# Kernel tuning notes

Measured on AMD Instinct MI355X. Metric: run time of the kernel, lower is better.

## Reference

```python
import jax, jax.numpy as jnp
import numpy as np

EPS_BN = 1e-5
EPS_W = 1e-8


def _bn(x, g, b, m, v):
    # x: [B, N, C]; params: [C] (inference-mode batchnorm)
    return g * (x - m) * jax.lax.rsqrt(v + EPS_BN) + b


def setup_inputs() -> dict:
    key = jax.random.key(0)
    ks = jax.random.split(key, 24)
    B, N, S = 16, 4096, 1024
    C1, C2 = 128, 256            # points1 / points2 channels
    CIN, COUT = C1 + C2, 128     # in_channel, out_channel

    def w(k, shape, std=0.02):
        return (jax.random.normal(k, shape, jnp.float32) * std)

    def bn_params(k, c):
        k1, k2, k3, k4 = jax.random.split(k, 4)
        return (1.0 + 0.1 * jax.random.normal(k1, (c,), jnp.float32),  # gamma
                0.1 * jax.random.normal(k2, (c,), jnp.float32),        # beta
                0.1 * jax.random.normal(k3, (c,), jnp.float32),        # running mean
                0.5 + jax.random.uniform(k4, (c,), jnp.float32))       # running var

    fg, fb, fm, fv = bn_params(ks[4], COUT)
    g1, b1, m1, v1 = bn_params(ks[5], COUT)
    g2, b2, m2, v2 = bn_params(ks[6], COUT)
    return {
        "xyz1": jax.random.uniform(ks[0], (B, N, 3), jnp.float32),
        "xyz2": jax.random.uniform(ks[1], (B, S, 3), jnp.float32),
        "points1": jax.random.normal(ks[2], (B, C1, N), jnp.float32),
        "points2": jax.random.normal(ks[3], (B, C2, S), jnp.float32),
        "fuse_w": w(ks[7], (COUT, CIN)), "fuse_b": jnp.zeros((COUT,), jnp.float32),
        "fuse_g": fg, "fuse_beta": fb, "fuse_m": fm, "fuse_v": fv,
        "c1_w": w(ks[8], (COUT, COUT)), "c1_b": jnp.zeros((COUT,), jnp.float32),
        "bn1_g": g1, "bn1_b": b1, "bn1_m": m1, "bn1_v": v1,
        "c2_w": w(ks[9], (COUT, COUT)), "c2_b": jnp.zeros((COUT,), jnp.float32),
        "bn2_g": g2, "bn2_b": b2, "bn2_m": m2, "bn2_v": v2,
    }


def reference(xyz1, xyz2, points1, points2,
              fuse_w, fuse_b, fuse_g, fuse_beta, fuse_m, fuse_v,
              c1_w, c1_b, bn1_g, bn1_b, bn1_m, bn1_v,
              c2_w, c2_b, bn2_g, bn2_b, bn2_m, bn2_v):
    B, N, _ = xyz1.shape
    pts1 = jnp.swapaxes(points1, 1, 2)   # [B, N, C1]
    pts2 = jnp.swapaxes(points2, 1, 2)   # [B, S, C2]

    # squared pairwise distances [B, N, S]
    dists = (jnp.sum(xyz1 ** 2, -1)[:, :, None]
             + jnp.sum(xyz2 ** 2, -1)[:, None, :]
             - 2.0 * jnp.einsum('bnc,bsc->bns', xyz1, xyz2))

    # 3 nearest neighbors (smallest distances)
    neg_d3, idx = jax.lax.top_k(-dists, 3)          # [B, N, 3]
    d3 = -neg_d3
    recip = 1.0 / (d3 + EPS_W)
    weight = recip / jnp.sum(recip, axis=2, keepdims=True)  # [B, N, 3]

    gathered = jax.vmap(lambda p, i: p[i])(pts2, idx)        # [B, N, 3, C2]
    interp = jnp.sum(gathered * weight[..., None], axis=2)   # [B, N, C2]

    x = jnp.concatenate([pts1, interp], axis=-1)             # [B, N, CIN]

    # fuse: 1x1 conv + BN + ReLU
    x = jax.nn.relu(_bn(jnp.einsum('bnc,oc->bno', x, fuse_w) + fuse_b,
                        fuse_g, fuse_beta, fuse_m, fuse_v))

    # residual block: conv-BN-ReLU -> conv-BN, add skip, ReLU
    h = jax.nn.relu(_bn(jnp.einsum('bnc,oc->bno', x, c1_w) + c1_b,
                        bn1_g, bn1_b, bn1_m, bn1_v))
    y = _bn(jnp.einsum('bnc,oc->bno', h, c2_w) + c2_b,
            bn2_g, bn2_b, bn2_m, bn2_v)
    out = jax.nn.relu(y + x)                                 # [B, N, COUT]
    return jnp.swapaxes(out, 1, 2)                           # [B, COUT, N]
```

## Files before the change

### kernel.cpp

```cpp
#include <hip/hip_runtime.h>
#include <hip/hip_bf16.h>

#define BB 16
#define NN 4096
#define SS 1024
#define C1 128
#define C2 256
#define CIN 384
#define CO 128

typedef __bf16 bf16x8 __attribute__((ext_vector_type(8)));
typedef float f32x4 __attribute__((ext_vector_type(4)));

__global__ __launch_bounds__(256) void knn_kernel(
    const float* __restrict__ xyz1, const float* __restrict__ xyz2,
    int* __restrict__ idx4, float* __restrict__ w4)
{
    __shared__ float4 pts[SS];
    const int b = blockIdx.y;
    const float* p2 = xyz2 + (size_t)b * SS * 3;
    for (int i = threadIdx.x; i < SS; i += 256) {
        float x = p2[i * 3 + 0], y = p2[i * 3 + 1], z = p2[i * 3 + 2];
        pts[i] = make_float4(x, y, z, x * x + y * y + z * z);
    }
    __syncthreads();

    const int n = blockIdx.x * 256 + threadIdx.x;
    const float* p1 = xyz1 + ((size_t)b * NN + n) * 3;
    const float x = p1[0], y = p1[1], z = p1[2];
    const float s1 = x * x + y * y + z * z;

    float d0 = 3.4e38f, d1 = 3.4e38f, d2 = 3.4e38f, d3 = 3.4e38f;
    int i0 = 0, i1 = 0, i2 = 0, i3 = 0;
    #pragma unroll 4
    for (int s = 0; s < SS; ++s) {
        float4 p = pts[s];
        float d = s1 + p.w - 2.0f * (x * p.x + y * p.y + z * p.z);
        bool lt0 = d < d0, lt1 = d < d1, lt2 = d < d2, lt3 = d < d3;
        float nd3 = lt2 ? d2 : (lt3 ? d : d3); int ni3 = lt2 ? i2 : (lt3 ? s : i3);
        float nd2 = lt1 ? d1 : (lt2 ? d : d2); int ni2 = lt1 ? i1 : (lt2 ? s : i2);
        float nd1 = lt0 ? d0 : (lt1 ? d : d1); int ni1 = lt0 ? i0 : (lt1 ? s : i1);
        d0 = lt0 ? d : d0;                     i0 = lt0 ? s : i0;
        d1 = nd1; i1 = ni1; d2 = nd2; i2 = ni2; d3 = nd3; i3 = ni3;
    }
    float r0 = 1.0f / (d0 + 1e-8f);
    float r1 = 1.0f / (d1 + 1e-8f);
    float r2 = 1.0f / (d2 + 1e-8f);
    float rs = r0 + r1 + r2;
    bool tie = (d2 == d3);
    size_t base = ((size_t)b * NN + n) * 4;
    idx4[base + 0] = i0; idx4[base + 1] = i1;
    idx4[base + 2] = i2; idx4[base + 3] = i3;
    w4[base + 0] = r0 / rs; w4[base + 1] = r1 / rs;
    w4[base + 2] = r2 / rs; w4[base + 3] = tie ? -1.0f : 0.0f;
}

__global__ __launch_bounds__(256) void p2t_kernel(
    const float* __restrict__ p2, float* __restrict__ p2t)
{
    __shared__ float tile[64][65];
    const int b = blockIdx.z;
    const int s0 = blockIdx.x * 64, c0 = blockIdx.y * 64;
    for (int i = threadIdx.x; i < 64 * 64; i += 256) {
        int s = i & 63, c = i >> 6;
        tile[c][s] = p2[((size_t)b * C2 + c0 + c) * SS + s0 + s];
    }
    __syncthreads();
    for (int i = threadIdx.x; i < 64 * 64; i += 256) {
        int c = i & 63, s = i >> 6;
        p2t[((size_t)b * SS + s0 + s) * C2 + c0 + c] = tile[c][s];
    }
}

__global__ __launch_bounds__(256) void tie_eval_kernel(
    const float* __restrict__ p2t, const float* __restrict__ points1,
    const int* __restrict__ idx4, float* __restrict__ w4,
    const float* __restrict__ fw, const float* __restrict__ fb,
    const float* __restrict__ fg, const float* __restrict__ fbt,
    const float* __restrict__ fm, const float* __restrict__ fv,
    const float* __restrict__ w1m, const float* __restrict__ b1,
    const float* __restrict__ g1, const float* __restrict__ bt1,
    const float* __restrict__ m1, const float* __restrict__ v1,
    const float* __restrict__ w2m, const float* __restrict__ b2,
    const float* __restrict__ g2, const float* __restrict__ bt2,
    const float* __restrict__ m2, const float* __restrict__ v2)
{
    __shared__ float Xs[4][2][CIN];
    __shared__ float XT[4][2][CO];
    __shared__ float Hs[4][2][CO];
    const int wave = threadIdx.x >> 6, lane = threadIdx.x & 63;
    const int n = blockIdx.x * 4 + wave;
    const int b = blockIdx.y;
    const size_t base = ((size_t)b * NN + n) * 4;
    if (w4[base + 3] != -1.0f) return;

    const int i0 = idx4[base + 0], i1 = idx4[base + 1];
    const int i2 = idx4[base + 2], i3 = idx4[base + 3];
    const float w0 = w4[base + 0], w1 = w4[base + 1], w2 = w4[base + 2];
    const float* P = p2t + (size_t)b * SS * C2;

    for (int c = lane; c < C1; c += 64) {
        float v = points1[((size_t)b * C1 + c) * NN + n];
        Xs[wave][0][c] = v; Xs[wave][1][c] = v;
    }
    for (int c = lane; c < C2; c += 64) {
        float f0 = P[(size_t)i0 * C2 + c], f1 = P[(size_t)i1 * C2 + c];
        float f2 = P[(size_t)i2 * C2 + c], f3 = P[(size_t)i3 * C2 + c];
        float bs = w0 * f0 + w1 * f1;
        Xs[wave][0][C1 + c] = bs + w2 * f2;
        Xs[wave][1][C1 + c] = bs + w2 * f3;
    }
    #pragma unroll
    for (int k = 0; k < 2; ++k) {
        int oc = lane + 64 * k;
        float alo = fb[oc], ahi = fb[oc];
        for (int c = 0; c < CIN; ++c) {
            float wv = fw[(size_t)oc * CIN + c];
            alo += wv * Xs[wave][0][c];
            ahi += wv * Xs[wave][1][c];
        }
        float s = fg[oc] * (1.0f / sqrtf(fv[oc] + 1e-5f));
        XT[wave][0][oc] = fmaxf(s * (alo - fm[oc]) + fbt[oc], 0.0f);
        XT[wave][1][oc] = fmaxf(s * (ahi - fm[oc]) + fbt[oc], 0.0f);
    }
    #pragma unroll
    for (int k = 0; k < 2; ++k) {
        int oc = lane + 64 * k;
        float alo = b1[oc], ahi = b1[oc];
        for (int c = 0; c < CO; ++c) {
            float wv = w1m[(size_t)oc * CO + c];
            alo += wv * XT[wave][0][c];
            ahi += wv * XT[wave][1][c];
        }
        float s = g1[oc] * (1.0f / sqrtf(v1[oc] + 1e-5f));
        Hs[wave][0][oc] = fmaxf(s * (alo - m1[oc]) + bt1[oc], 0.0f);
        Hs[wave][1][oc] = fmaxf(s * (ahi - m1[oc]) + bt1[oc], 0.0f);
    }
    float e = 0.0f;
    #pragma unroll
    for (int k = 0; k < 2; ++k) {
        int oc = lane + 64 * k;
        float alo = b2[oc], ahi = b2[oc];
        for (int c = 0; c < CO; ++c) {
            float wv = w2m[(size_t)oc * CO + c];
            alo += wv * Hs[wave][0][c];
            ahi += wv * Hs[wave][1][c];
        }
        float s = g2[oc] * (1.0f / sqrtf(v2[oc] + 1e-5f));
        float olo = fmaxf(s * (alo - m2[oc]) + bt2[oc] + XT[wave][0][oc], 0.0f);
        float ohi = fmaxf(s * (ahi - m2[oc]) + bt2[oc] + XT[wave][1][oc], 0.0f);
        e = fmaxf(e, fabsf(olo - ohi));
    }
    for (int off = 32; off; off >>= 1) e = fmaxf(e, __shfl_xor(e, off));
    if (lane == 0) {
        if (e > 0.085f) { w4[base + 3] = 0.0f; }
        else { w4[base + 2] = 0.5f * w2; w4[base + 3] = 0.5f * w2; }
    }
}

__global__ __launch_bounds__(256) void buildx_kernel(
    const float* __restrict__ points1,
    const float* __restrict__ p2t,
    const int* __restrict__ idx4, const float* __restrict__ w4,
    float* __restrict__ X)
{
    __shared__ float t1[128][66];
    const int b = blockIdx.y;
    const int n0 = blockIdx.x * 64;
    for (int i = threadIdx.x; i < 128 * 64; i += 256) {
        int j = i & 63, c = i >> 6;
        t1[c][j] = points1[((size_t)b * C1 + c) * NN + n0 + j];
    }
    __syncthreads();
    for (int i = threadIdx.x; i < 128 * 64; i += 256) {
        int c = i & 127, j = i >> 7;
        X[((size_t)b * NN + n0 + j) * CIN + c] = t1[c][j];
    }
    for (int i = threadIdx.x; i < 64 * C2; i += 256) {
        int c = i & 255, j = i >> 8;
        int n = n0 + j;
        size_t ib = ((size_t)b * NN + n) * 4;
        int s0 = idx4[ib + 0], s1 = idx4[ib + 1];
        int s2 = idx4[ib + 2], s3 = idx4[ib + 3];
        float w0 = w4[ib + 0], w1 = w4[ib + 1];
        float w2 = w4[ib + 2], w3 = w4[ib + 3];
        const float* base = p2t + (size_t)b * SS * C2;
        float v = w0 * base[(size_t)s0 * C2 + c]
                + w1 * base[(size_t)s1 * C2 + c]
                + w2 * base[(size_t)s2 * C2 + c]
                + w3 * base[(size_t)s3 * C2 + c];
        X[((size_t)b * NN + n) * CIN + C1 + c] = v;
    }
}

template<int K, int MODE>
__global__ __launch_bounds__(256) void gemm_bn_kernel(
    const float* __restrict__ A,
    const float* __restrict__ W,
    const float* __restrict__ cb,  const float* __restrict__ gg,
    const float* __restrict__ bbta, const float* __restrict__ mm,
    const float* __restrict__ vv,
    const float* __restrict__ skip,
    float* __restrict__ out)
{
    __shared__ __attribute__((aligned(16))) __hip_bfloat16 wh[128 * 40];
    __shared__ __attribute__((aligned(16))) __hip_bfloat16 wl[128 * 40];
    __shared__ float s_s[128], s_t[128];
    const int tid = threadIdx.x;
    if (tid < 128) {
        float s = gg[tid] * (1.0f / sqrtf(vv[tid] + 1e-5f));
        float t = (cb[tid] - mm[tid]) * s + bbta[tid];
        s_s[tid] = s; s_t[tid] = t;
    }
    const int wave = tid >> 6, lane = tid & 63;
    const int m = lane & 15, q = lane >> 4;
    const size_t r0 = (size_t)blockIdx.x * 64 + wave * 16;

    f32x4 acc[8] = {};
    const float* arow = A + (r0 + m) * K + q * 8;

    for (int kk = 0; kk < K; kk += 32) {
        __syncthreads();
        int c = tid;
        #pragma unroll
        for (int rep = 0; rep < 2; ++rep, c += 256) {
            int row = c >> 2, qq = c & 3;
            const float4 wa = *(const float4*)&W[(size_t)row * K + kk + qq * 8];
            const float4 wb = *(const float4*)&W[(size_t)row * K + kk + qq * 8 + 4];
            float wf[8] = {wa.x, wa.y, wa.z, wa.w, wb.x, wb.y, wb.z, wb.w};
            bf16x8 vh, vl;
            #pragma unroll
            for (int t = 0; t < 8; ++t) {
                __bf16 h = (__bf16)wf[t];
                vh[t] = h;
                vl[t] = (__bf16)(wf[t] - (float)h);
            }
            *(bf16x8*)&wh[row * 40 + qq * 8] = vh;
            *(bf16x8*)&wl[row * 40 + qq * 8] = vl;
        }
        __syncthreads();
        const float4 aa = *(const float4*)(arow + kk);
        const float4 ab = *(const float4*)(arow + kk + 4);
        float af[8] = {aa.x, aa.y, aa.z, aa.w, ab.x, ab.y, ab.z, ab.w};
        bf16x8 a_hi, a_lo;
        #pragma unroll
        for (int t = 0; t < 8; ++t) {
            __bf16 h = (__bf16)af[t];
            a_hi[t] = h;
            a_lo[t] = (__bf16)(af[t] - (float)h);
        }
        #pragma unroll
        for (int ot = 0; ot < 8; ++ot) {
            bf16x8 bh = *(const bf16x8*)&wh[(ot * 16 + m) * 40 + q * 8];
            bf16x8 bl = *(const bf16x8*)&wl[(ot * 16 + m) * 40 + q * 8];
            acc[ot] = __builtin_amdgcn_mfma_f32_16x16x32_bf16(a_hi, bh, acc[ot], 0, 0, 0);
            acc[ot] = __builtin_amdgcn_mfma_f32_16x16x32_bf16(a_lo, bh, acc[ot], 0, 0, 0);
            acc[ot] = __builtin_amdgcn_mfma_f32_16x16x32_bf16(a_hi, bl, acc[ot], 0, 0, 0);
        }
    }

    #pragma unroll
    for (int ot = 0; ot < 8; ++ot) {
        int col = ot * 16 + m;
        float sc = s_s[col], sh = s_t[col];
        #pragma unroll
        for (int r = 0; r < 4; ++r) {
            size_t row = r0 + q * 4 + r;
            float val = acc[ot][r] * sc + sh;
            if (MODE == 0) {
                val = fmaxf(val, 0.0f);
                out[row * 128 + col] = val;
            } else {
                val += skip[row * 128 + col];
                val = fmaxf(val, 0.0f);
                int bidx = (int)(row >> 12);
                int n = (int)(row & 4095);
                out[((size_t)bidx * 128 + col) * NN + n] = val;
            }
        }
    }
}

extern "C" void kernel_launch(void* const* d_in, const int* in_sizes, int n_in,
                              void* d_out, int out_size, void* d_ws, size_t ws_size,
                              hipStream_t stream) {
    const float* xyz1    = (const float*)d_in[0];
    const float* xyz2    = (const float*)d_in[1];
    const float* points1 = (const float*)d_in[2];
    const float* points2 = (const float*)d_in[3];
    const float* fuse_w  = (const float*)d_in[4];
    const float* fuse_b  = (const float*)d_in[5];
    const float* fuse_g  = (const float*)d_in[6];
    const float* fuse_bt = (const float*)d_in[7];
    const float* fuse_m  = (const float*)d_in[8];
    const float* fuse_v  = (const float*)d_in[9];
    const float* c1_w    = (const float*)d_in[10];
    const float* c1_b    = (const float*)d_in[11];
    const float* bn1_g   = (const float*)d_in[12];
    const float* bn1_b   = (const float*)d_in[13];
    const float* bn1_m   = (const float*)d_in[14];
    const float* bn1_v   = (const float*)d_in[15];
    const float* c2_w    = (const float*)d_in[16];
    const float* c2_b    = (const float*)d_in[17];
    const float* bn2_g   = (const float*)d_in[18];
    const float* bn2_b   = (const float*)d_in[19];
    const float* bn2_m   = (const float*)d_in[20];
    const float* bn2_v   = (const float*)d_in[21];

    char* ws = (char*)d_ws;
    int*   idx4 = (int*)(ws);
    float* w4   = (float*)(ws + 1048576);
    float* p2t  = (float*)(ws + 2097152);
    float* X    = (float*)(ws + 18874368);
    float* Y0   = (float*)(ws + 119537664);
    float* H    = (float*)(ws + 153092096);

    knn_kernel<<<dim3(NN / 256, BB), 256, 0, stream>>>(xyz1, xyz2, idx4, w4);
    p2t_kernel<<<dim3(SS / 64, C2 / 64, BB), 256, 0, stream>>>(points2, p2t);
    tie_eval_kernel<<<dim3(NN / 4, BB), 256, 0, stream>>>(
        p2t, points1, idx4, w4,
        fuse_w, fuse_b, fuse_g, fuse_bt, fuse_m, fuse_v,
        c1_w, c1_b, bn1_g, bn1_b, bn1_m, bn1_v,
        c2_w, c2_b, bn2_g, bn2_b, bn2_m, bn2_v);
    buildx_kernel<<<dim3(NN / 64, BB), 256, 0, stream>>>(points1, p2t, idx4, w4, X);

    const int mblocks = (BB * NN) / 64;
    gemm_bn_kernel<CIN, 0><<<mblocks, 256, 0, stream>>>(
        X, fuse_w, fuse_b, fuse_g, fuse_bt, fuse_m, fuse_v, nullptr, Y0);
    gemm_bn_kernel<CO, 0><<<mblocks, 256, 0, stream>>>(
        Y0, c1_w, c1_b, bn1_g, bn1_b, bn1_m, bn1_v, nullptr, H);
    gemm_bn_kernel<CO, 1><<<mblocks, 256, 0, stream>>>(
        H, c2_w, c2_b, bn2_g, bn2_b, bn2_m, bn2_v, Y0, (float*)d_out);
}
```

Measured before the change: 374.6 us.

## Pre-split operands into bf16 hi/lo, double GEMM row tile, coalesce transposed output

Weights are split into bf16 hi/lo pairs once in a new prep kernel, and the activations X, Y0 and H are stored as bf16 hi/lo pairs, so the GEMMs no longer convert fp32 to bf16 on every tile. Each wave now computes 32 rows instead of 16, which reuses each LDS weight fragment twice. The final GEMM transposes its output through shared memory so the [B,C,N] writes are coalesced. The intermediate traffic stays the same size (two bf16 halves per fp32 value), but it adds an extra launch and more accumulator registers, which may lower occupancy.

```diff
diff --git a/kernel.cpp b/kernel.cpp
--- a/kernel.cpp
+++ b/kernel.cpp
@@ -72,6 +72,22 @@
     }
 }
 
+__global__ __launch_bounds__(256) void wprep_kernel(
+    const float* __restrict__ fw, const float* __restrict__ w1,
+    const float* __restrict__ w2,
+    __bf16* __restrict__ Whf, __bf16* __restrict__ Wlf,
+    __bf16* __restrict__ Wh1, __bf16* __restrict__ Wl1,
+    __bf16* __restrict__ Wh2, __bf16* __restrict__ Wl2)
+{
+    int t = blockIdx.x * 256 + threadIdx.x;
+    float v; __bf16 *oh, *ol; int idx;
+    if (t < 49152)      { idx = t;         v = fw[idx]; oh = Whf; ol = Wlf; }
+    else if (t < 65536) { idx = t - 49152; v = w1[idx]; oh = Wh1; ol = Wl1; }
+    else                { idx = t - 65536; v = w2[idx]; oh = Wh2; ol = Wl2; }
+    __bf16 h = (__bf16)v;
+    oh[idx] = h; ol[idx] = (__bf16)(v - (float)h);
+}
+
 __global__ __launch_bounds__(256) void tie_eval_kernel(
     const float* __restrict__ p2t, const float* __restrict__ points1,
     const int* __restrict__ idx4, float* __restrict__ w4,
@@ -162,7 +178,7 @@
     const float* __restrict__ points1,
     const float* __restrict__ p2t,
     const int* __restrict__ idx4, const float* __restrict__ w4,
-    float* __restrict__ X)
+    __bf16* __restrict__ Xh, __bf16* __restrict__ Xl)
 {
     __shared__ float t1[128][66];
     const int b = blockIdx.y;
@@ -174,7 +190,10 @@
     __syncthreads();
     for (int i = threadIdx.x; i < 128 * 64; i += 256) {
         int c = i & 127, j = i >> 7;
-        X[((size_t)b * NN + n0 + j) * CIN + c] = t1[c][j];
+        float v = t1[c][j];
+        __bf16 h = (__bf16)v;
+        size_t o = ((size_t)b * NN + n0 + j) * CIN + c;
+        Xh[o] = h; Xl[o] = (__bf16)(v - (float)h);
     }
     for (int i = threadIdx.x; i < 64 * C2; i += 256) {
         int c = i & 255, j = i >> 8;
@@ -189,23 +208,27 @@
                 + w1 * base[(size_t)s1 * C2 + c]
                 + w2 * base[(size_t)s2 * C2 + c]
                 + w3 * base[(size_t)s3 * C2 + c];
-        X[((size_t)b * NN + n) * CIN + C1 + c] = v;
+        __bf16 h = (__bf16)v;
+        size_t o = ((size_t)b * NN + n) * CIN + C1 + c;
+        Xh[o] = h; Xl[o] = (__bf16)(v - (float)h);
     }
 }
 
 template<int K, int MODE>
 __global__ __launch_bounds__(256) void gemm_bn_kernel(
-    const float* __restrict__ A,
-    const float* __restrict__ W,
+    const __bf16* __restrict__ Ah, const __bf16* __restrict__ Al,
+    const __bf16* __restrict__ Wh, const __bf16* __restrict__ Wl,
     const float* __restrict__ cb,  const float* __restrict__ gg,
     const float* __restrict__ bbta, const float* __restrict__ mm,
     const float* __restrict__ vv,
-    const float* __restrict__ skip,
-    float* __restrict__ out)
-{
-    __shared__ __attribute__((aligned(16))) __hip_bfloat16 wh[128 * 40];
-    __shared__ __attribute__((aligned(16))) __hip_bfloat16 wl[128 * 40];
+    const __bf16* __restrict__ skiph, const __bf16* __restrict__ skipl,
+    __bf16* __restrict__ outh, __bf16* __restrict__ outl,
+    float* __restrict__ outf)
+{
+    __shared__ __attribute__((aligned(16))) __bf16 wls_h[128 * 40];
+    __shared__ __attribute__((aligned(16))) __bf16 wls_l[128 * 40];
     __shared__ float s_s[128], s_t[128];
+    __shared__ float tile[32][132];
     const int tid = threadIdx.x;
     if (tid < 128) {
         float s = gg[tid] * (1.0f / sqrtf(vv[tid] + 1e-5f));
@@ -214,68 +237,85 @@
     }
     const int wave = tid >> 6, lane = tid & 63;
     const int m = lane & 15, q = lane >> 4;
-    const size_t r0 = (size_t)blockIdx.x * 64 + wave * 16;
-
-    f32x4 acc[8] = {};
-    const float* arow = A + (r0 + m) * K + q * 8;
-
+    const size_t r0 = (size_t)blockIdx.x * 128 + wave * 32;
+
+    f32x4 acc[2][8] = {};
+    const __bf16* pAh = Ah + (r0 + m) * (size_t)K + q * 8;
+    const __bf16* pAl = Al + (r0 + m) * (size_t)K + q * 8;
+
+    const int wrow = tid >> 1, whf = tid & 1;
     for (int kk = 0; kk < K; kk += 32) {
         __syncthreads();
-        int c = tid;
-        #pragma unroll
-        for (int rep = 0; rep < 2; ++rep, c += 256) {
-            int row = c >> 2, qq = c & 3;
-            const float4 wa = *(const float4*)&W[(size_t)row * K + kk + qq * 8];
-            const float4 wb = *(const float4*)&W[(size_t)row * K + kk + qq * 8 + 4];
-            float wf[8] = {wa.x, wa.y, wa.z, wa.w, wb.x, wb.y, wb.z, wb.w};
-            bf16x8 vh, vl;
-            #pragma unroll
-            for (int t = 0; t < 8; ++t) {
-                __bf16 h = (__bf16)wf[t];
-                vh[t] = h;
-                vl[t] = (__bf16)(wf[t] - (float)h);
-            }
-            *(bf16x8*)&wh[row * 40 + qq * 8] = vh;
-            *(bf16x8*)&wl[row * 40 + qq * 8] = vl;
+        {
+            size_t g = (size_t)wrow * K + kk + whf * 16;
+            int lo = wrow * 40 + whf * 16;
+            *(uint4*)&wls_h[lo]     = *(const uint4*)&Wh[g];
+            *(uint4*)&wls_h[lo + 8] = *(const uint4*)&Wh[g + 8];
+            *(uint4*)&wls_l[lo]     = *(const uint4*)&Wl[g];
+            *(uint4*)&wls_l[lo + 8] = *(const uint4*)&Wl[g + 8];
         }
         __syncthreads();
-        const float4 aa = *(const float4*)(arow + kk);
-        const float4 ab = *(const float4*)(arow + kk + 4);
-        float af[8] = {aa.x, aa.y, aa.z, aa.w, ab.x, ab.y, ab.z, ab.w};
-        bf16x8 a_hi, a_lo;
-        #pragma unroll
-        for (int t = 0; t < 8; ++t) {
-            __bf16 h = (__bf16)af[t];
-            a_hi[t] = h;
-            a_lo[t] = (__bf16)(af[t] - (float)h);
-        }
+        bf16x8 ah0 = *(const bf16x8*)(pAh + kk);
+        bf16x8 al0 = *(const bf16x8*)(pAl + kk);
+        bf16x8 ah1 = *(const bf16x8*)(pAh + 16 * (size_t)K + kk);
+        bf16x8 al1 = *(const bf16x8*)(pAl + 16 * (size_t)K + kk);
         #pragma unroll
         for (int ot = 0; ot < 8; ++ot) {
-            bf16x8 bh = *(const bf16x8*)&wh[(ot * 16 + m) * 40 + q * 8];
-            bf16x8 bl = *(const bf16x8*)&wl[(ot * 16 + m) * 40 + q * 8];
-            acc[ot] = __builtin_amdgcn_mfma_f32_16x16x32_bf16(a_hi, bh, acc[ot], 0, 0, 0);
-            acc[ot] = __builtin_amdgcn_mfma_f32_16x16x32_bf16(a_lo, bh, acc[ot], 0, 0, 0);
-            acc[ot] = __builtin_amdgcn_mfma_f32_16x16x32_bf16(a_hi, bl, acc[ot], 0, 0, 0);
-        }
-    }
-
-    #pragma unroll
-    for (int ot = 0; ot < 8; ++ot) {
-        int col = ot * 16 + m;
-        float sc = s_s[col], sh = s_t[col];
+            bf16x8 bh = *(const bf16x8*)&wls_h[(ot * 16 + m) * 40 + q * 8];
+            bf16x8 bl = *(const bf16x8*)&wls_l[(ot * 16 + m) * 40 + q * 8];
+            acc[0][ot] = __builtin_amdgcn_mfma_f32_16x16x32_bf16(ah0, bh, acc[0][ot], 0, 0, 0);
+            acc[0][ot] = __builtin_amdgcn_mfma_f32_16x16x32_bf16(al0, bh, acc[0][ot], 0, 0, 0);
+            acc[0][ot] = __builtin_amdgcn_mfma_f32_16x16x32_bf16(ah0, bl, acc[0][ot], 0, 0, 0);
+            acc[1][ot] = __builtin_amdgcn_mfma_f32_16x16x32_bf16(ah1, bh, acc[1][ot], 0, 0, 0);
+            acc[1][ot] = __builtin_amdgcn_mfma_f32_16x16x32_bf16(al1, bh, acc[1][ot], 0, 0, 0);
+            acc[1][ot] = __builtin_amdgcn_mfma_f32_16x16x32_bf16(ah1, bl, acc[1][ot], 0, 0, 0);
+        }
+    }
+
+    if (MODE == 0) {
         #pragma unroll
-        for (int r = 0; r < 4; ++r) {
-            size_t row = r0 + q * 4 + r;
-            float val = acc[ot][r] * sc + sh;
-            if (MODE == 0) {
-                val = fmaxf(val, 0.0f);
-                out[row * 128 + col] = val;
-            } else {
-                val += skip[row * 128 + col];
-                val = fmaxf(val, 0.0f);
-                int bidx = (int)(row >> 12);
-                int n = (int)(row & 4095);
-                out[((size_t)bidx * 128 + col) * NN + n] = val;
+        for (int rt = 0; rt < 2; ++rt) {
+            #pragma unroll
+            for (int ot = 0; ot < 8; ++ot) {
+                int col = ot * 16 + m;
+                float sc = s_s[col], sh = s_t[col];
+                #pragma unroll
+                for (int r = 0; r < 4; ++r) {
+                    size_t row = r0 + rt * 16 + q * 4 + r;
+                    float val = fmaxf(acc[rt][ot][r] * sc + sh, 0.0f);
+                    __bf16 h = (__bf16)val;
+                    outh[row * 128 + col] = h;
+                    outl[row * 128 + col] = (__bf16)(val - (float)h);
+                }
+            }
+        }
+    } else {
+        const int bidx = (int)(((size_t)blockIdx.x * 128) >> 12);
+        const int nbase = (int)(((size_t)blockIdx.x * 128) & 4095);
+        for (int cc = 0; cc < 4; ++cc) {
+            __syncthreads();
+            #pragma unroll
+            for (int oo = 0; oo < 2; ++oo) {
+                int ot = cc * 2 + oo;
+                int col = ot * 16 + m;
+                float sc = s_s[col], sh = s_t[col];
+                #pragma unroll
+                for (int rt = 0; rt < 2; ++rt) {
+                    #pragma unroll
+                    for (int r = 0; r < 4; ++r) {
+                        int lrow = wave * 32 + rt * 16 + q * 4 + r;
+                        size_t row = (size_t)blockIdx.x * 128 + lrow;
+                        float val = acc[rt][ot][r] * sc + sh;
+                        val += (float)skiph[row * 128 + col] + (float)skipl[row * 128 + col];
+                        val = fmaxf(val, 0.0f);
+                        tile[oo * 16 + m][lrow] = val;
+                    }
+                }
+            }
+            __syncthreads();
+            for (int c2 = tid >> 7; c2 < 32; c2 += 2) {
+                int nn_ = tid & 127;
+                outf[((size_t)bidx * 128 + cc * 32 + c2) * NN + nbase + nn_] = tile[c2][nn_];
             }
         }
     }
@@ -308,27 +348,41 @@
     const float* bn2_v   = (const float*)d_in[21];
 
     char* ws = (char*)d_ws;
-    int*   idx4 = (int*)(ws);
-    float* w4   = (float*)(ws + 1048576);
-    float* p2t  = (float*)(ws + 2097152);
-    float* X    = (float*)(ws + 18874368);
-    float* Y0   = (float*)(ws + 119537664);
-    float* H    = (float*)(ws + 153092096);
+    int*    idx4 = (int*)(ws);
+    float*  w4   = (float*)(ws + 1048576);
+    float*  p2t  = (float*)(ws + 2097152);
+    __bf16* Xh   = (__bf16*)(ws + 18874368);
+    __bf16* Xl   = (__bf16*)(ws + 69206016);
+    __bf16* Y0h  = (__bf16*)(ws + 119537664);
+    __bf16* Y0l  = (__bf16*)(ws + 136314880);
+    __bf16* Hh   = (__bf16*)(ws + 153092096);
+    __bf16* Hl   = (__bf16*)(ws + 169869312);
+    __bf16* Whf  = (__bf16*)(ws + 186646528);
+    __bf16* Wlf  = (__bf16*)(ws + 186744832);
+    __bf16* Wh1  = (__bf16*)(ws + 186843136);
+    __bf16* Wl1  = (__bf16*)(ws + 186875904);
+    __bf16* Wh2  = (__bf16*)(ws + 186908672);
+    __bf16* Wl2  = (__bf16*)(ws + 186941440);
 
     knn_kernel<<<dim3(NN / 256, BB), 256, 0, stream>>>(xyz1, xyz2, idx4, w4);
     p2t_kernel<<<dim3(SS / 64, C2 / 64, BB), 256, 0, stream>>>(points2, p2t);
+    wprep_kernel<<<320, 256, 0, stream>>>(fuse_w, c1_w, c2_w,
+                                          Whf, Wlf, Wh1, Wl1, Wh2, Wl2);
     tie_eval_kernel<<<dim3(NN / 4, BB), 256, 0, stream>>>(
         p2t, points1, idx4, w4,
         fuse_w, fuse_b, fuse_g, fuse_bt, fuse_m, fuse_v,
         c1_w, c1_b, bn1_g, bn1_b, bn1_m, bn1_v,
         c2_w, c2_b, bn2_g, bn2_b, bn2_m, bn2_v);
-    buildx_kernel<<<dim3(NN / 64, BB), 256, 0, stream>>>(points1, p2t, idx4, w4, X);
-
-    const int mblocks = (BB * NN) / 64;
-    gemm_bn_kernel<CIN, 0><<<mblocks, 256, 0, stream>>>(
-        X, fuse_w, fuse_b, fuse_g, fuse_bt, fuse_m, fuse_v, nullptr, Y0);
-    gemm_bn_kernel<CO, 0><<<mblocks, 256, 0, stream>>>(
-        Y0, c1_w, c1_b, bn1_g, bn1_b, bn1_m, bn1_v, nullptr, H);
-    gemm_bn_kernel<CO, 1><<<mblocks, 256, 0, stream>>>(
-        H, c2_w, c2_b, bn2_g, bn2_b, bn2_m, bn2_v, Y0, (float*)d_out);
-}
+    buildx_kernel<<<dim3(NN / 64, BB), 256, 0, stream>>>(points1, p2t, idx4, w4, Xh, Xl);
+
+    const int gblocks = (BB * NN) / 128;
+    gemm_bn_kernel<CIN, 0><<<gblocks, 256, 0, stream>>>(
+        Xh, Xl, Whf, Wlf, fuse_b, fuse_g, fuse_bt, fuse_m, fuse_v,
+        nullptr, nullptr, Y0h, Y0l, nullptr);
+    gemm_bn_kernel<CO, 0><<<gblocks, 256, 0, stream>>>(
+        Y0h, Y0l, Wh1, Wl1, c1_b, bn1_g, bn1_b, bn1_m, bn1_v,
+        nullptr, nullptr, Hh, Hl, nullptr);
+    gemm_bn_kernel<CO, 1><<<gblocks, 256, 0, stream>>>(
+        Hh, Hl, Wh2, Wl2, c2_b, bn2_g, bn2_b, bn2_m, bn2_v,
+        Y0h, Y0l, nullptr, nullptr, (float*)d_out);
+}
```

Measured after the change: 371.1 us. No clear change (-0.9%).
